# Performance work log

Measured on AMD Instinct MI355X. Metric: run time of the kernel, lower is better.

The kernel has to match this reference:

```python
import jax, jax.numpy as jnp
import numpy as np

D = 1024
K = 256
B = 8192


def setup_inputs() -> dict:
    key = jax.random.key(0)
    kx, kw, kd, kp = jax.random.split(key, 4)
    x = jax.random.normal(kx, (B, D), dtype=jnp.float32)
    # scale weights ~1/sqrt(d) so the 11-matmul chain stays numerically sane
    Ws = jax.random.normal(kw, (10, D, D), dtype=jnp.float32) / jnp.sqrt(jnp.float32(D))
    W_dec = jax.random.normal(kd, (D, K), dtype=jnp.float32) / jnp.sqrt(jnp.float32(K))
    perm = jax.random.randint(kp, (K,), 0, D, dtype=jnp.int64)
    return {"x": x, "Ws": Ws, "W_dec": W_dec, "perm": perm}


def reference(x, Ws, W_dec, perm):
    # torch nn.Linear(d,d,bias=False): y = x @ W.T
    # source applies fc1..fc9, then fc9 AGAIN, then fc10 (11 matmuls, 10 weights)
    order = list(range(9)) + [8, 9]
    h = x
    for i in order:
        h = h @ Ws[i].T  # [B, D]
    y = h[:, perm]        # vectorized gather, replaces per-row python loop [B, K]
    out = y @ W_dec.T     # fc_decode: [B, D]
    return out
```

## Files before the change

kernel.cpp:

```cpp
#include <hip/hip_runtime.h>
#include <stdint.h>
#include <stddef.h>

typedef __bf16 bf16;
typedef __bf16 bf16x8 __attribute__((ext_vector_type(8)));
typedef float f32x4 __attribute__((ext_vector_type(4)));

__device__ __forceinline__ void global_to_lds16(const void* g, void* l) {
  const __attribute__((address_space(1))) unsigned* gp =
      reinterpret_cast<const __attribute__((address_space(1))) unsigned*>(
          reinterpret_cast<uintptr_t>(g));
  __attribute__((address_space(3))) unsigned* lp =
      reinterpret_cast<__attribute__((address_space(3))) unsigned*>(
          reinterpret_cast<uintptr_t>(l));
  __builtin_amdgcn_global_load_lds(gp, lp, 16, 0, 0);
}

__global__ __launch_bounds__(256) void cvt_f32_bf16(const float* __restrict__ src,
                                                    bf16* __restrict__ dst) {
  int i = (blockIdx.x * 256 + threadIdx.x) * 8;
  float4 a = *(const float4*)(src + i);
  float4 b = *(const float4*)(src + i + 4);
  bf16x8 o;
  o[0] = (bf16)a.x; o[1] = (bf16)a.y; o[2] = (bf16)a.z; o[3] = (bf16)a.w;
  o[4] = (bf16)b.x; o[5] = (bf16)b.y; o[6] = (bf16)b.z; o[7] = (bf16)b.w;
  *(bf16x8*)(dst + i) = o;
}

struct CvtBatch { const float* src[5]; bf16* dst[5]; };
__global__ __launch_bounds__(256) void cvt_f32_bf16_batch(CvtBatch cb) {
  const float* src = cb.src[blockIdx.z];
  bf16* dst = cb.dst[blockIdx.z];
  int i = (blockIdx.x * 256 + threadIdx.x) * 8;
  float4 a = *(const float4*)(src + i);
  float4 b = *(const float4*)(src + i + 4);
  bf16x8 o;
  o[0] = (bf16)a.x; o[1] = (bf16)a.y; o[2] = (bf16)a.z; o[3] = (bf16)a.w;
  o[4] = (bf16)b.x; o[5] = (bf16)b.y; o[6] = (bf16)b.z; o[7] = (bf16)b.w;
  *(bf16x8*)(dst + i) = o;
}

struct TrBatch { const float* src[6]; bf16* dst[6]; };
__global__ __launch_bounds__(256) void transpose_cvt_batch(TrBatch tb) {
  const float* __restrict__ src = tb.src[blockIdx.z];
  bf16* __restrict__ dst = tb.dst[blockIdx.z];
  __shared__ bf16 tile[64][65];
  const int bx = blockIdx.x * 64;
  const int by = blockIdx.y * 64;
  const int tx = threadIdx.x & 63;
  const int ty4 = threadIdx.x >> 6;
#pragma unroll
  for (int rr = 0; rr < 16; rr++) {
    int row = ty4 * 16 + rr;
    tile[row][tx] = (bf16)src[(size_t)(by + row) * 1024 + bx + tx];
  }
  __syncthreads();
#pragma unroll
  for (int rr = 0; rr < 16; rr++) {
    int row = ty4 * 16 + rr;
    dst[(size_t)(bx + row) * 1024 + by + tx] = tile[tx][row];
  }
}

__global__ __launch_bounds__(256) void normalize_perm(const int* __restrict__ raw,
                                                      int* __restrict__ pout) {
  __shared__ int nz;
  if (threadIdx.x == 0) nz = 0;
  __syncthreads();
  if (threadIdx.x < 128) {
    if (raw[2 * threadIdx.x + 1] != 0) atomicAdd(&nz, 1);
  }
  __syncthreads();
  int k = threadIdx.x;
  pout[k] = (nz == 0) ? raw[2 * k] : raw[k];
}

__global__ __launch_bounds__(256) void zero_f32(float* __restrict__ p) {
  int i = (blockIdx.x * 256 + threadIdx.x) * 4;
  *(float4*)(p + i) = make_float4(0.f, 0.f, 0.f, 0.f);
}

__global__ __launch_bounds__(256) void scatter_g(const float* __restrict__ Wdec,
                                                 const int* __restrict__ perm,
                                                 float* __restrict__ G) {
  int idx = blockIdx.x * 256 + threadIdx.x;
  int j = idx >> 8, k = idx & 255;
  atomicAdd(G + (size_t)j * 1024 + perm[k], Wdec[(size_t)j * 256 + k]);
}

struct GemmBatch { const bf16* A[6]; const bf16* B[6]; bf16* C[6]; };

__global__ __launch_bounds__(256) void gemm64_nt(GemmBatch bt) {
  const bf16* __restrict__ A = bt.A[blockIdx.z];
  const bf16* __restrict__ B = bt.B[blockIdx.z];
  bf16* __restrict__ C = bt.C[blockIdx.z];

  __shared__ bf16 As[64 * 32];
  __shared__ bf16 Bs[64 * 32];

  const int tid = threadIdx.x;
  const int wave = tid >> 6, lane = tid & 63;
  const int quad = lane >> 4, l16 = lane & 15;
  const int rowBase = blockIdx.y * 64;
  const int colBase = blockIdx.x * 64;
  const int waveM = (wave >> 1) * 32, waveN = (wave & 1) * 32;

  const int e = tid * 8;
  const int sr = e >> 5, sc = e & 31;
  const bf16* Ag = A + (size_t)(rowBase + sr) * 1024 + sc;
  const bf16* Bg = B + (size_t)(colBase + sr) * 1024 + sc;
  char* AsB = (char*)As + wave * 1024;
  char* BsB = (char*)Bs + wave * 1024;

  f32x4 acc[2][2] = {};

  for (int k0 = 0; k0 < 1024; k0 += 32) {
    global_to_lds16(Ag + k0, AsB);
    global_to_lds16(Bg + k0, BsB);
    __syncthreads();
    bf16x8 af[2], bfr[2];
#pragma unroll
    for (int mi = 0; mi < 2; mi++)
      af[mi] = *(const bf16x8*)(As + (waveM + mi * 16 + l16) * 32 + quad * 8);
#pragma unroll
    for (int ni = 0; ni < 2; ni++)
      bfr[ni] = *(const bf16x8*)(Bs + (waveN + ni * 16 + l16) * 32 + quad * 8);
#pragma unroll
    for (int mi = 0; mi < 2; mi++)
#pragma unroll
      for (int ni = 0; ni < 2; ni++)
        acc[mi][ni] = __builtin_amdgcn_mfma_f32_16x16x32_bf16(af[mi], bfr[ni],
                                                              acc[mi][ni], 0, 0, 0);
    __syncthreads();
  }

  bf16* Cb = C + (size_t)(rowBase + waveM) * 1024 + colBase + waveN;
#pragma unroll
  for (int mi = 0; mi < 2; mi++)
#pragma unroll
    for (int ni = 0; ni < 2; ni++)
#pragma unroll
      for (int r = 0; r < 4; r++)
        Cb[(size_t)(mi * 16 + quad * 4 + r) * 1024 + ni * 16 + l16] =
            (bf16)acc[mi][ni][r];
}

__global__ __launch_bounds__(256) void gemm128_nt_f32(const bf16* __restrict__ A,
                                                      const bf16* __restrict__ B,
                                                      float* __restrict__ C) {
  __shared__ bf16 As[128 * 32];
  __shared__ bf16 Bs[128 * 32];

  const int tid = threadIdx.x;
  const int wave = tid >> 6, lane = tid & 63;
  const int quad = lane >> 4, l16 = lane & 15;
  const int rowBase = blockIdx.y * 128;
  const int colBase = blockIdx.x * 128;
  const int waveM = (wave >> 1) * 64, waveN = (wave & 1) * 64;

  const int e = tid * 8;
  const int sr = e >> 5, sc = e & 31;
  const bf16* Ag0 = A + (size_t)(rowBase + sr) * 1024 + sc;
  const bf16* Ag1 = Ag0 + (size_t)64 * 1024;
  const bf16* Bg0 = B + (size_t)(colBase + sr) * 1024 + sc;
  const bf16* Bg1 = Bg0 + (size_t)64 * 1024;
  char* AsB0 = (char*)As + wave * 1024;
  char* AsB1 = AsB0 + 4096;
  char* BsB0 = (char*)Bs + wave * 1024;
  char* BsB1 = BsB0 + 4096;

  f32x4 acc[4][4] = {};

  for (int k0 = 0; k0 < 1024; k0 += 32) {
    global_to_lds16(Ag0 + k0, AsB0);
    global_to_lds16(Ag1 + k0, AsB1);
    global_to_lds16(Bg0 + k0, BsB0);
    global_to_lds16(Bg1 + k0, BsB1);
    __syncthreads();
    bf16x8 af[4], bfr[4];
#pragma unroll
    for (int mi = 0; mi < 4; mi++)
      af[mi] = *(const bf16x8*)(As + (waveM + mi * 16 + l16) * 32 + quad * 8);
#pragma unroll
    for (int ni = 0; ni < 4; ni++)
      bfr[ni] = *(const bf16x8*)(Bs + (waveN + ni * 16 + l16) * 32 + quad * 8);
#pragma unroll
    for (int mi = 0; mi < 4; mi++)
#pragma unroll
      for (int ni = 0; ni < 4; ni++)
        acc[mi][ni] = __builtin_amdgcn_mfma_f32_16x16x32_bf16(af[mi], bfr[ni],
                                                              acc[mi][ni], 0, 0, 0);
    __syncthreads();
  }

  float* Cb = C + (size_t)(rowBase + waveM) * 1024 + colBase + waveN;
#pragma unroll
  for (int mi = 0; mi < 4; mi++)
#pragma unroll
    for (int ni = 0; ni < 4; ni++)
#pragma unroll
      for (int r = 0; r < 4; r++)
        Cb[(size_t)(mi * 16 + quad * 4 + r) * 1024 + ni * 16 + l16] =
            acc[mi][ni][r];
}

extern "C" void kernel_launch(void* const* d_in, const int* in_sizes, int n_in,
                              void* d_out, int out_size, void* d_ws, size_t ws_size,
                              hipStream_t stream) {
  const float* x    = (const float*)d_in[0];
  const float* Wsrc = (const float*)d_in[1];
  const float* Wdec = (const float*)d_in[2];
  const int*   praw = (const int*)d_in[3];
  float* out = (float*)d_out;

  constexpr size_t MAT  = 1024ull * 1024ull;
  constexpr size_t SLOT = 2ull * 1024 * 1024;

  char* ws = (char*)d_ws;
  bf16* Wrm[5];
  for (int i = 0; i < 5; i++) Wrm[i] = (bf16*)(ws + (size_t)i * SLOT);
  bf16* Wt[6];
  for (int i = 0; i < 6; i++) Wt[i] = (bf16*)(ws + (size_t)(5 + i) * SLOT);
  bf16* Gbf = (bf16*)(ws + 11 * SLOT);
  bf16* xbf = (bf16*)(ws + 12 * SLOT);
  bf16* P[6];
  for (int i = 0; i < 6; i++) P[i] = (bf16*)(ws + (size_t)(20 + i) * SLOT);
  bf16* Q[3];
  for (int i = 0; i < 3; i++) Q[i] = (bf16*)(ws + (size_t)(26 + i) * SLOT);
  bf16* Rb = (bf16*)(ws + 29 * SLOT);
  bf16* Fb = (bf16*)(ws + 30 * SLOT);
  float* Gf32 = (float*)(ws + 20 * SLOT);
  int* permN = (int*)(ws + 31 * SLOT);

  CvtBatch cb;
  const int rmIdx[5] = {1, 3, 5, 7, 8};
  for (int i = 0; i < 5; i++) { cb.src[i] = Wsrc + (size_t)rmIdx[i] * MAT; cb.dst[i] = Wrm[i]; }
  cvt_f32_bf16_batch<<<dim3(512, 1, 5), 256, 0, stream>>>(cb);

  TrBatch tb;
  const int trIdx[6] = {0, 2, 4, 6, 8, 9};
  for (int i = 0; i < 6; i++) { tb.src[i] = Wsrc + (size_t)trIdx[i] * MAT; tb.dst[i] = Wt[i]; }
  transpose_cvt_batch<<<dim3(16, 16, 6), 256, 0, stream>>>(tb);

  cvt_f32_bf16<<<4096, 256, 0, stream>>>(x, xbf);

  zero_f32<<<1024, 256, 0, stream>>>(Gf32);
  normalize_perm<<<1, 256, 0, stream>>>(praw, permN);
  scatter_g<<<1024, 256, 0, stream>>>(Wdec, permN, Gf32);
  cvt_f32_bf16<<<512, 256, 0, stream>>>(Gf32, Gbf);

  GemmBatch L1;
  const bf16* l1a[6] = {Gbf, Wt[4], Wrm[3], Wt[2], Wrm[1], Wt[0]};
  const bf16* l1b[6] = {Wt[5], Wrm[4], Wt[3], Wrm[2], Wt[1], Wrm[0]};
  for (int i = 0; i < 6; i++) { L1.A[i] = l1a[i]; L1.B[i] = l1b[i]; L1.C[i] = P[i]; }
  gemm64_nt<<<dim3(16, 16, 6), 256, 0, stream>>>(L1);

  GemmBatch L2;
  const bf16* l2a[3] = {P[0], P[3], P[5]};
  const bf16* l2b[3] = {P[1], P[2], P[4]};
  for (int i = 0; i < 3; i++) { L2.A[i] = l2a[i]; L2.B[i] = l2b[i]; L2.C[i] = Q[i]; }
  gemm64_nt<<<dim3(16, 16, 3), 256, 0, stream>>>(L2);

  GemmBatch L3{};
  L3.A[0] = Q[0]; L3.B[0] = Q[1]; L3.C[0] = Rb;
  gemm64_nt<<<dim3(16, 16, 1), 256, 0, stream>>>(L3);

  GemmBatch L4{};
  L4.A[0] = Rb; L4.B[0] = Q[2]; L4.C[0] = Fb;
  gemm64_nt<<<dim3(16, 16, 1), 256, 0, stream>>>(L4);

  gemm128_nt_f32<<<dim3(8, 64), 256, 0, stream>>>(xbf, Fb, out);

  (void)in_sizes; (void)n_in; (void)out_size; (void)ws_size;
}
```

Measured before the change: 239.9 us.

## Fuse all preprocessing conversions and decode-matrix scatter into one kernel launch

Merges seven small prep kernels (weight conversion, transposes, x conversion, zeroing, perm normalization, scatter, G conversion) into a single block-indexed prep kernel. The scatter of W_dec into G now happens per row in shared memory with LDS atomics, so the global fp32 G buffer, its zeroing, and the separate conversion pass are no longer needed. This removes several launch gaps and a global-atomic round trip. The cost is a heterogeneous kernel whose branches share one shared-memory allocation.

Result: faster. 222.5 us (-7.3%).

```diff
diff --git a/kernel.cpp b/kernel.cpp
--- a/kernel.cpp
+++ b/kernel.cpp
@@ -16,76 +16,79 @@
   __builtin_amdgcn_global_load_lds(gp, lp, 16, 0, 0);
 }
 
-__global__ __launch_bounds__(256) void cvt_f32_bf16(const float* __restrict__ src,
-                                                    bf16* __restrict__ dst) {
-  int i = (blockIdx.x * 256 + threadIdx.x) * 8;
-  float4 a = *(const float4*)(src + i);
-  float4 b = *(const float4*)(src + i + 4);
-  bf16x8 o;
-  o[0] = (bf16)a.x; o[1] = (bf16)a.y; o[2] = (bf16)a.z; o[3] = (bf16)a.w;
-  o[4] = (bf16)b.x; o[5] = (bf16)b.y; o[6] = (bf16)b.z; o[7] = (bf16)b.w;
-  *(bf16x8*)(dst + i) = o;
-}
-
-struct CvtBatch { const float* src[5]; bf16* dst[5]; };
-__global__ __launch_bounds__(256) void cvt_f32_bf16_batch(CvtBatch cb) {
-  const float* src = cb.src[blockIdx.z];
-  bf16* dst = cb.dst[blockIdx.z];
-  int i = (blockIdx.x * 256 + threadIdx.x) * 8;
-  float4 a = *(const float4*)(src + i);
-  float4 b = *(const float4*)(src + i + 4);
-  bf16x8 o;
-  o[0] = (bf16)a.x; o[1] = (bf16)a.y; o[2] = (bf16)a.z; o[3] = (bf16)a.w;
-  o[4] = (bf16)b.x; o[5] = (bf16)b.y; o[6] = (bf16)b.z; o[7] = (bf16)b.w;
-  *(bf16x8*)(dst + i) = o;
-}
-
-struct TrBatch { const float* src[6]; bf16* dst[6]; };
-__global__ __launch_bounds__(256) void transpose_cvt_batch(TrBatch tb) {
-  const float* __restrict__ src = tb.src[blockIdx.z];
-  bf16* __restrict__ dst = tb.dst[blockIdx.z];
-  __shared__ bf16 tile[64][65];
-  const int bx = blockIdx.x * 64;
-  const int by = blockIdx.y * 64;
-  const int tx = threadIdx.x & 63;
-  const int ty4 = threadIdx.x >> 6;
-#pragma unroll
-  for (int rr = 0; rr < 16; rr++) {
-    int row = ty4 * 16 + rr;
-    tile[row][tx] = (bf16)src[(size_t)(by + row) * 1024 + bx + tx];
+struct PrepArgs {
+  const float* cvt_src[5]; bf16* cvt_dst[5];
+  const float* tr_src[6];  bf16* tr_dst[6];
+  const float* x; bf16* xbf;
+  const float* Wdec; const int* praw; bf16* Gbf;
+};
+
+__global__ __launch_bounds__(256) void prep_all(PrepArgs p) {
+  __shared__ alignas(16) char smem[64 * 65 * 2];
+  const int b = blockIdx.x;
+  const int tid = threadIdx.x;
+
+  if (b < 2560) {
+    const int m = b >> 9, blk = b & 511;
+    const float* __restrict__ src = p.cvt_src[m];
+    bf16* __restrict__ dst = p.cvt_dst[m];
+    const int i = (blk * 256 + tid) * 8;
+    float4 a = *(const float4*)(src + i);
+    float4 c = *(const float4*)(src + i + 4);
+    bf16x8 o;
+    o[0] = (bf16)a.x; o[1] = (bf16)a.y; o[2] = (bf16)a.z; o[3] = (bf16)a.w;
+    o[4] = (bf16)c.x; o[5] = (bf16)c.y; o[6] = (bf16)c.z; o[7] = (bf16)c.w;
+    *(bf16x8*)(dst + i) = o;
+  } else if (b < 4096) {
+    const int t = b - 2560;
+    const int m = t >> 8, r = t & 255;
+    const float* __restrict__ src = p.tr_src[m];
+    bf16* __restrict__ dst = p.tr_dst[m];
+    bf16(*tile)[65] = reinterpret_cast<bf16(*)[65]>(smem);
+    const int bx = (r & 15) * 64;
+    const int by = (r >> 4) * 64;
+    const int tx = tid & 63;
+    const int ty4 = tid >> 6;
+#pragma unroll
+    for (int rr = 0; rr < 16; rr++) {
+      int row = ty4 * 16 + rr;
+      tile[row][tx] = (bf16)src[(size_t)(by + row) * 1024 + bx + tx];
+    }
+    __syncthreads();
+#pragma unroll
+    for (int rr = 0; rr < 16; rr++) {
+      int row = ty4 * 16 + rr;
+      dst[(size_t)(bx + row) * 1024 + by + tx] = tile[tx][row];
+    }
+  } else if (b < 8192) {
+    const int blk = b - 4096;
+    const int i = (blk * 256 + tid) * 8;
+    float4 a = *(const float4*)(p.x + i);
+    float4 c = *(const float4*)(p.x + i + 4);
+    bf16x8 o;
+    o[0] = (bf16)a.x; o[1] = (bf16)a.y; o[2] = (bf16)a.z; o[3] = (bf16)a.w;
+    o[4] = (bf16)c.x; o[5] = (bf16)c.y; o[6] = (bf16)c.z; o[7] = (bf16)c.w;
+    *(bf16x8*)(p.xbf + i) = o;
+  } else {
+    const int j = b - 8192;
+    float* row = (float*)smem;
+    int* perm_l = (int*)(smem + 4096);
+    int* nzp = (int*)(smem + 4096 + 1024);
+#pragma unroll
+    for (int c = 0; c < 4; c++) row[tid * 4 + c] = 0.f;
+    if (tid == 0) *nzp = 0;
+    __syncthreads();
+    if (tid < 128 && p.praw[2 * tid + 1] != 0) atomicOr(nzp, 1);
+    __syncthreads();
+    const int is64 = (*nzp == 0);
+    perm_l[tid] = is64 ? p.praw[2 * tid] : p.praw[tid];
+    __syncthreads();
+    atomicAdd(&row[perm_l[tid]], p.Wdec[(size_t)j * 256 + tid]);
+    __syncthreads();
+#pragma unroll
+    for (int c = 0; c < 4; c++)
+      p.Gbf[(size_t)j * 1024 + tid * 4 + c] = (bf16)row[tid * 4 + c];
   }
-  __syncthreads();
-#pragma unroll
-  for (int rr = 0; rr < 16; rr++) {
-    int row = ty4 * 16 + rr;
-    dst[(size_t)(bx + row) * 1024 + by + tx] = tile[tx][row];
-  }
-}
-
-__global__ __launch_bounds__(256) void normalize_perm(const int* __restrict__ raw,
-                                                      int* __restrict__ pout) {
-  __shared__ int nz;
-  if (threadIdx.x == 0) nz = 0;
-  __syncthreads();
-  if (threadIdx.x < 128) {
-    if (raw[2 * threadIdx.x + 1] != 0) atomicAdd(&nz, 1);
-  }
-  __syncthreads();
-  int k = threadIdx.x;
-  pout[k] = (nz == 0) ? raw[2 * k] : raw[k];
-}
-
-__global__ __launch_bounds__(256) void zero_f32(float* __restrict__ p) {
-  int i = (blockIdx.x * 256 + threadIdx.x) * 4;
-  *(float4*)(p + i) = make_float4(0.f, 0.f, 0.f, 0.f);
-}
-
-__global__ __launch_bounds__(256) void scatter_g(const float* __restrict__ Wdec,
-                                                 const int* __restrict__ perm,
-                                                 float* __restrict__ G) {
-  int idx = blockIdx.x * 256 + threadIdx.x;
-  int j = idx >> 8, k = idx & 255;
-  atomicAdd(G + (size_t)j * 1024 + perm[k], Wdec[(size_t)j * 256 + k]);
 }
 
 struct GemmBatch { const bf16* A[6]; const bf16* B[6]; bf16* C[6]; };
@@ -229,25 +232,14 @@
   for (int i = 0; i < 3; i++) Q[i] = (bf16*)(ws + (size_t)(26 + i) * SLOT);
   bf16* Rb = (bf16*)(ws + 29 * SLOT);
   bf16* Fb = (bf16*)(ws + 30 * SLOT);
-  float* Gf32 = (float*)(ws + 20 * SLOT);
-  int* permN = (int*)(ws + 31 * SLOT);
-
-  CvtBatch cb;
+
+  PrepArgs pa;
   const int rmIdx[5] = {1, 3, 5, 7, 8};
-  for (int i = 0; i < 5; i++) { cb.src[i] = Wsrc + (size_t)rmIdx[i] * MAT; cb.dst[i] = Wrm[i]; }
-  cvt_f32_bf16_batch<<<dim3(512, 1, 5), 256, 0, stream>>>(cb);
-
-  TrBatch tb;
+  for (int i = 0; i < 5; i++) { pa.cvt_src[i] = Wsrc + (size_t)rmIdx[i] * MAT; pa.cvt_dst[i] = Wrm[i]; }
   const int trIdx[6] = {0, 2, 4, 6, 8, 9};
-  for (int i = 0; i < 6; i++) { tb.src[i] = Wsrc + (size_t)trIdx[i] * MAT; tb.dst[i] = Wt[i]; }
-  transpose_cvt_batch<<<dim3(16, 16, 6), 256, 0, stream>>>(tb);
-
-  cvt_f32_bf16<<<4096, 256, 0, stream>>>(x, xbf);
-
-  zero_f32<<<1024, 256, 0, stream>>>(Gf32);
-  normalize_perm<<<1, 256, 0, stream>>>(praw, permN);
-  scatter_g<<<1024, 256, 0, stream>>>(Wdec, permN, Gf32);
-  cvt_f32_bf16<<<512, 256, 0, stream>>>(Gf32, Gbf);
+  for (int i = 0; i < 6; i++) { pa.tr_src[i] = Wsrc + (size_t)trIdx[i] * MAT; pa.tr_dst[i] = Wt[i]; }
+  pa.x = x; pa.xbf = xbf; pa.Wdec = Wdec; pa.praw = praw; pa.Gbf = Gbf;
+  prep_all<<<dim3(9216), 256, 0, stream>>>(pa);
 
   GemmBatch L1;
   const bf16* l1a[6] = {Gbf, Wt[4], Wrm[3], Wt[2], Wrm[1], Wt[0]};
```
